# Optimization experiments

Hardware: AMD Instinct MI355X
Metric: run time of the kernel (lower is better)

Reference implementation:

```python
import jax, jax.numpy as jnp
import numpy as np

E = 8      # num_experts
A = 128    # angle feature size = input_size - 4
TGT = 3    # target size
HID = 16   # expert MLP hidden / latent / main GRU hidden
OUT = 128  # motion decoder output size
B = 64
W = 128
F = A + TGT + 1  # 132
BN_EPS = 1e-5


def _gru_layer(x, Wih, Whh, bih, bhh):
    # x: (B, T, I); Wih: (3H, I); Whh: (3H, H). PyTorch GRU equations.
    xW = jnp.einsum('bti,gi->btg', x, Wih) + bih  # precompute input gates (B,T,3H)
    H = Whh.shape[1]

    def step(h, xw):
        gh = h @ Whh.T + bhh
        ir, iz, inn = jnp.split(xw, 3, axis=-1)
        hr, hz, hn = jnp.split(gh, 3, axis=-1)
        r = jax.nn.sigmoid(ir + hr)
        z = jax.nn.sigmoid(iz + hz)
        n = jnp.tanh(inn + r * hn)
        h_new = (1.0 - z) * n + z * h
        return h_new, h_new

    h0 = jnp.zeros((x.shape[0], H), x.dtype)
    _, ys = jax.lax.scan(step, h0, jnp.swapaxes(xW, 0, 1))
    return jnp.swapaxes(ys, 0, 1)  # (B, T, H)


def _expert_mlp(x, om, w1, b1, w2, b2, g, bt):
    # Blend expert weights per-sample, then matvec; fused as one einsum (same math).
    h = jnp.einsum('bi,be,eih->bh', x, om, w1) + om @ b1
    # BatchNorm1d, training-mode batch statistics (biased variance), then ELU
    m = h.mean(0)
    v = h.var(0)
    h = jax.nn.elu(g * (h - m) * jax.lax.rsqrt(v + BN_EPS) + bt)
    return jnp.einsum('bh,be,eho->bo', h, om, w2) + om @ b2


def _forward(Local, Remote,
             gW_ih0, gW_hh0, gb_ih0, gb_hh0, gW_ih1, gW_hh1, gb_ih1, gb_hh1,
             ae_w1, ae_b1, ae_w2, ae_b2, ae_g, ae_bt,
             md_w1, md_b1, md_w2, md_b2, md_g, md_bt,
             mW_ih0, mW_hh0, mb_ih0, mb_hh0, mW_ih1, mW_hh1, mb_ih1, mb_hh1):
    Bn, Wn, _ = Local.shape
    LA = Local[..., :A]
    RA = Remote[..., :A]
    LT = Local[..., A:A + TGT]
    RT = Remote[..., A:A + TGT]
    Scale = Remote[..., A + TGT]  # (B, W)

    def gate(t):
        h = _gru_layer(t, gW_ih0, gW_hh0, gb_ih0, gb_hh0)
        h = _gru_layer(h, gW_ih1, gW_hh1, gb_ih1, gb_hh1)
        return jax.nn.softmax(h, axis=-1)

    Lo = gate(LT)  # (B, W, E)
    Ro = gate(RT)

    ZL = _expert_mlp(LA.reshape(-1, A), Lo.reshape(-1, E), ae_w1, ae_b1, ae_w2, ae_b2, ae_g, ae_bt)
    ZR = _expert_mlp(RA.reshape(-1, A), Ro.reshape(-1, E), ae_w1, ae_b1, ae_w2, ae_b2, ae_g, ae_bt)
    Z = (ZL + ZR).reshape(Bn, Wn, HID)

    Z = _gru_layer(Z, mW_ih0, mW_hh0, mb_ih0, mb_hh0)
    Z = _gru_layer(Z, mW_ih1, mW_hh1, mb_ih1, mb_hh1)
    Z = Z[:, -1]  # (B, HID)

    dec_in = jnp.concatenate([Z, Scale[:, -1:]], axis=-1)  # (B, HID+1)
    return _expert_mlp(dec_in, Ro[:, -1], md_w1, md_b1, md_w2, md_b2, md_g, md_bt)


def setup_inputs() -> dict:
    key = jax.random.key(0)
    ks = iter(jax.random.split(key, 40))

    def u(shape, bound):
        return jax.random.uniform(next(ks), shape, jnp.float32, -bound, bound)

    d = {}
    d['Local'] = jax.random.normal(next(ks), (B, W, F), jnp.float32)
    d['Remote'] = jax.random.normal(next(ks), (B, W, F), jnp.float32)

    def gru_params(pref, isz, hsz):
        bd = 1.0 / np.sqrt(hsz)
        d[pref + 'W_ih0'] = u((3 * hsz, isz), bd)
        d[pref + 'W_hh0'] = u((3 * hsz, hsz), bd)
        d[pref + 'b_ih0'] = u((3 * hsz,), bd)
        d[pref + 'b_hh0'] = u((3 * hsz,), bd)
        d[pref + 'W_ih1'] = u((3 * hsz, hsz), bd)
        d[pref + 'W_hh1'] = u((3 * hsz, hsz), bd)
        d[pref + 'b_ih1'] = u((3 * hsz,), bd)
        d[pref + 'b_hh1'] = u((3 * hsz,), bd)

    gru_params('g', TGT, E)    # gating GRU: 2 layers, hidden = num_experts
    gru_params('m', HID, HID)  # main GRU: 2 layers, hidden = 16

    def expert(pref, isz, hsz, osz):
        b1 = float(np.sqrt(6.0 / (isz * hsz)))
        b2 = float(np.sqrt(6.0 / (hsz * osz)))
        d[pref + '_w1'] = u((E, isz, hsz), b1)
        d[pref + '_b1'] = jnp.zeros((E, hsz), jnp.float32)
        d[pref + '_w2'] = u((E, hsz, osz), b2)
        d[pref + '_b2'] = jnp.zeros((E, osz), jnp.float32)
        d[pref + '_g'] = jnp.ones((hsz,), jnp.float32)
        d[pref + '_bt'] = jnp.zeros((hsz,), jnp.float32)

    expert('ae', A, HID, HID)        # angle encoder
    expert('md', HID + 1, HID, OUT)  # motion decoder
    return d


def reference(Local, Remote,
              gW_ih0, gW_hh0, gb_ih0, gb_hh0, gW_ih1, gW_hh1, gb_ih1, gb_hh1,
              ae_w1, ae_b1, ae_w2, ae_b2, ae_g, ae_bt,
              md_w1, md_b1, md_w2, md_b2, md_g, md_bt,
              mW_ih0, mW_hh0, mb_ih0, mb_hh0, mW_ih1, mW_hh1, mb_ih1, mb_hh1):
    return _forward(Local, Remote,
                    gW_ih0, gW_hh0, gb_ih0, gb_hh0, gW_ih1, gW_hh1, gb_ih1, gb_hh1,
                    ae_w1, ae_b1, ae_w2, ae_b2, ae_g, ae_bt,
                    md_w1, md_b1, md_w2, md_b2, md_g, md_bt,
                    mW_ih0, mW_hh0, mb_ih0, mb_hh0, mW_ih1, mW_hh1, mb_ih1, mb_hh1)
```

## Files before the change

### kernel.cpp

```cpp
#include <hip/hip_runtime.h>
#include <cstdint>
#include <cstddef>

#define DEV __device__ __forceinline__

typedef float f2 __attribute__((ext_vector_type(2)));

constexpr float L2E = 1.4426950408889634f;
constexpr float T2E = 2.8853900817779268f;

DEV float readlanef(float v, int l) {
    return __uint_as_float(__builtin_amdgcn_readlane(__float_as_uint(v), l));
}
DEV float fsig2(float y)  { return __builtin_amdgcn_rcpf(1.0f + __builtin_amdgcn_exp2f(-y)); }
DEV float ftanh2(float y) { return 1.0f - 2.0f * __builtin_amdgcn_rcpf(1.0f + __builtin_amdgcn_exp2f(y)); }

constexpr size_t ACC   = 0;
constexpr size_t LO    = 128;
constexpr size_t RO    = LO + 65536;
constexpr size_t HBUF  = RO + 65536;
constexpr size_t ZLAST = HBUF + 262144;

__global__ __launch_bounds__(64, 1) void k1_gate(
    const float* __restrict__ Local, const float* __restrict__ Remote,
    const float* __restrict__ Wih0, const float* __restrict__ Whh0,
    const float* __restrict__ bih0, const float* __restrict__ bhh0,
    const float* __restrict__ Wih1, const float* __restrict__ Whh1,
    const float* __restrict__ bih1, const float* __restrict__ bhh1,
    float* __restrict__ ws)
{
    const int tid = threadIdx.x;
    const int j = tid & 7;
    const int layer = (tid >> 3) & 1;
    const int blk = blockIdx.x;
    const int track = blk >> 6;
    const int b = blk & 63;
    if (blk == 0) ws[ACC + tid] = 0.f;

    __shared__ float xwg[128][24];
    __shared__ float h1all[128][9];

    const float* __restrict__ src = track ? Remote : Local;
    for (int t = tid; t < 128; t += 64) {
        const float* p = src + ((size_t)b * 128 + t) * 132 + 128;
        float x0 = p[0], x1 = p[1], x2 = p[2];
#pragma unroll
        for (int u = 0; u < 24; ++u) {
            float a = bih0[u];
            a = fmaf(Wih0[u * 3 + 0], x0, a);
            a = fmaf(Wih0[u * 3 + 1], x1, a);
            a = fmaf(Wih0[u * 3 + 2], x2, a);
            xwg[t][u] = a * (u < 16 ? L2E : T2E);
        }
    }

    const float* __restrict__ Wlo = layer ? Wih1 : Whh0;
    const float mhi = layer ? 1.f : 0.f;
    const float m0f = layer ? 0.f : 1.f;
    f2 wr2[8], wz2[8], wc2[8];
#pragma unroll
    for (int m = 0; m < 4; ++m) {
        wr2[m].x = L2E * Wlo[j * 8 + 2 * m];
        wr2[m].y = L2E * Wlo[j * 8 + 2 * m + 1];
        wz2[m].x = L2E * Wlo[(8 + j) * 8 + 2 * m];
        wz2[m].y = L2E * Wlo[(8 + j) * 8 + 2 * m + 1];
        wc2[m].x = T2E * Wlo[(16 + j) * 8 + 2 * m];
        wc2[m].y = T2E * Wlo[(16 + j) * 8 + 2 * m + 1];
        wr2[4 + m].x = mhi * L2E * Whh1[j * 8 + 2 * m];
        wr2[4 + m].y = mhi * L2E * Whh1[j * 8 + 2 * m + 1];
        wz2[4 + m].x = mhi * L2E * Whh1[(8 + j) * 8 + 2 * m];
        wz2[4 + m].y = mhi * L2E * Whh1[(8 + j) * 8 + 2 * m + 1];
        wc2[4 + m].x = mhi * T2E * Whh1[(16 + j) * 8 + 2 * m];
        wc2[4 + m].y = mhi * T2E * Whh1[(16 + j) * 8 + 2 * m + 1];
    }
    const float base_r  = L2E * (layer ? (bih1[j] + bhh1[j])         : bhh0[j]);
    const float base_z  = L2E * (layer ? (bih1[8 + j] + bhh1[8 + j]) : bhh0[8 + j]);
    const float base_in = T2E * (layer ? bih1[16 + j]                : 0.f);
    const float base_dn = T2E * (layer ? bhh1[16 + j]                : bhh0[16 + j]);
    __syncthreads();

    float hown = 0.f;
    float p0 = xwg[0][j], p1 = xwg[0][8 + j], p2 = xwg[0][16 + j];
#pragma unroll 1
    for (int t = 0; t <= 128; ++t) {
        int tn = t < 127 ? t + 1 : 127;
        float q0 = xwg[tn][j], q1 = xwg[tn][8 + j], q2 = xwg[tn][16 + j];
        f2 vb2[8];
#pragma unroll
        for (int m = 0; m < 8; ++m) {
            vb2[m].x = readlanef(hown, 2 * m);
            vb2[m].y = readlanef(hown, 2 * m + 1);
        }
        f2 srE = wr2[0] * vb2[0], srO = wr2[1] * vb2[1];
        f2 szE = wz2[0] * vb2[0], szO = wz2[1] * vb2[1];
#pragma unroll
        for (int m = 2; m < 8; m += 2) {
            srE += wr2[m] * vb2[m];     srO += wr2[m + 1] * vb2[m + 1];
            szE += wz2[m] * vb2[m];     szO += wz2[m + 1] * vb2[m + 1];
        }
        f2 scA = wc2[0] * vb2[0], scB = wc2[1] * vb2[1];
        f2 scC = wc2[4] * vb2[4], scD = wc2[5] * vb2[5];
#pragma unroll
        for (int m = 2; m < 4; m += 2) {
            scA += wc2[m] * vb2[m];     scB += wc2[m + 1] * vb2[m + 1];
            scC += wc2[4 + m] * vb2[4 + m]; scD += wc2[5 + m] * vb2[5 + m];
        }
        f2 sr = srE + srO, sz = szE + szO;
        f2 scL = scA + scB, scH = scC + scD;
        float ar = fmaf(m0f, p0, base_r) + sr.x + sr.y;
        float az = fmaf(m0f, p1, base_z) + sz.x + sz.y;
        float ac_lo = scL.x + scL.y;
        float ac_hi = scH.x + scH.y;
        float r = fsig2(ar);
        float z = fsig2(az);
        float in_ = layer ? (base_in + ac_lo) : p2;
        float dn  = base_dn + (layer ? ac_hi : ac_lo);
        float n = ftanh2(fmaf(r, dn, in_));
        float hnew = fmaf(z, hown - n, n);
        bool act = layer ? (t >= 1) : (t < 128);
        hown = act ? hnew : hown;
        if (tid >= 8 && tid < 16) h1all[t ? t - 1 : 0][j] = hown;
        p0 = q0; p1 = q1; p2 = q2;
    }
    __syncthreads();

    float* __restrict__ outp = ws + (track ? RO : LO);
    for (int t = tid; t < 128; t += 64) {
        float vv[8];
#pragma unroll
        for (int k = 0; k < 8; ++k) vv[k] = h1all[t][k];
        float mx = vv[0];
#pragma unroll
        for (int k = 1; k < 8; ++k) mx = fmaxf(mx, vv[k]);
        float ssum = 0.f;
#pragma unroll
        for (int k = 0; k < 8; ++k) { vv[k] = __expf(vv[k] - mx); ssum += vv[k]; }
        float inv = __builtin_amdgcn_rcpf(ssum);
        size_t base = ((size_t)b * 128 + t) * 8;
        float4 o0 = make_float4(vv[0] * inv, vv[1] * inv, vv[2] * inv, vv[3] * inv);
        float4 o1 = make_float4(vv[4] * inv, vv[5] * inv, vv[6] * inv, vv[7] * inv);
        *(float4*)(outp + base) = o0;
        *(float4*)(outp + base + 4) = o1;
    }
}

__global__ __launch_bounds__(256) void k2_expert1(
    const float* __restrict__ Local, const float* __restrict__ Remote,
    const float* __restrict__ ae_w1, const float* __restrict__ ae_b1,
    float* __restrict__ ws)
{
    const int blk = blockIdx.x;
    const int track = blk >> 7;
    const int n0 = (blk & 127) * 64;
    const float* __restrict__ X = track ? Remote : Local;
    const float* __restrict__ om = ws + (track ? RO : LO);

    __shared__ __align__(16) float xsh[64 * 132];
    __shared__ __align__(16) float wsh[16 * 1060];
    __shared__ float omsh[64][8];
    __shared__ float b1sh[128];
    __shared__ float red[32];
    const int tid = threadIdx.x;

    for (int i = tid; i < 2048; i += 256) {
        int r = i >> 5, q = i & 31;
        ((float4*)&xsh[r * 132])[q] = ((const float4*)(X + (size_t)(n0 + r) * 132))[q];
    }
    for (int i4 = tid; i4 < 4096; i4 += 256) {
        float4 v = ((const float4*)ae_w1)[i4];
        int i = i4 * 4;
#pragma unroll
        for (int c = 0; c < 4; ++c) {
            int ii = i + c;
            int h = ii & 15, kk = (ii >> 4) & 127, e = ii >> 11;
            float vc = c == 0 ? v.x : c == 1 ? v.y : c == 2 ? v.z : v.w;
            wsh[h * 1060 + e * 132 + kk] = vc;
        }
    }
    for (int i = tid; i < 512; i += 256) omsh[i >> 3][i & 7] = om[(size_t)(n0 + (i >> 3)) * 8 + (i & 7)];
    for (int i = tid; i < 128; i += 256) b1sh[i] = ae_b1[i];
    if (tid < 32) red[tid] = 0.f;
    __syncthreads();

    const int hh = tid & 15, rg = tid >> 4;
    float acc[4][8];
#pragma unroll
    for (int r = 0; r < 4; ++r)
#pragma unroll
        for (int e = 0; e < 8; ++e) acc[r][e] = 0.f;

#pragma unroll 4
    for (int kq = 0; kq < 32; ++kq) {
        float4 xv[4], wv[8];
#pragma unroll
        for (int r = 0; r < 4; ++r) xv[r] = *(const float4*)&xsh[(rg * 4 + r) * 132 + kq * 4];
#pragma unroll
        for (int e = 0; e < 8; ++e) wv[e] = *(const float4*)&wsh[hh * 1060 + e * 132 + kq * 4];
#pragma unroll
        for (int r = 0; r < 4; ++r)
#pragma unroll
            for (int e = 0; e < 8; ++e) {
                float a = acc[r][e];
                a = fmaf(xv[r].x, wv[e].x, a);
                a = fmaf(xv[r].y, wv[e].y, a);
                a = fmaf(xv[r].z, wv[e].z, a);
                a = fmaf(xv[r].w, wv[e].w, a);
                acc[r][e] = a;
            }
    }

    float s = 0.f, s2 = 0.f;
    float* __restrict__ hout = ws + HBUF + (size_t)track * 131072;
#pragma unroll
    for (int r = 0; r < 4; ++r) {
        int row = rg * 4 + r;
        float hv = 0.f;
#pragma unroll
        for (int e = 0; e < 8; ++e) hv = fmaf(omsh[row][e], acc[r][e] + b1sh[e * 16 + hh], hv);
        hout[(size_t)(n0 + row) * 16 + hh] = hv;
        s += hv; s2 += hv * hv;
    }
    __syncthreads();
    atomicAdd(&red[hh], s);
    atomicAdd(&red[16 + hh], s2);
    __syncthreads();
    if (tid < 32) atomicAdd(&ws[ACC + track * 32 + tid], red[tid]);
}

__global__ __launch_bounds__(256, 1) void k34_fused(
    const float* __restrict__ ae_w2, const float* __restrict__ ae_b2,
    const float* __restrict__ ae_g, const float* __restrict__ ae_bt,
    const float* __restrict__ mWih0, const float* __restrict__ mbih0,
    const float* __restrict__ Whh0, const float* __restrict__ bhh0,
    const float* __restrict__ Wih1, const float* __restrict__ Whh1,
    const float* __restrict__ bih1, const float* __restrict__ bhh1,
    float* __restrict__ ws)
{
    const int s = blockIdx.x;
    const int tid = threadIdx.x;

    __shared__ float stat[4][16];
    __shared__ float omsh[2][128][8];
    __shared__ __align__(16) float w2t[16 * 132];
    __shared__ float b2sh[128];
    __shared__ __align__(16) float actsh[2][128][16];
    __shared__ __align__(16) float zsh[128][20];
    __shared__ __align__(16) float wihsh[48][20];
    __shared__ float bihsh[48];
    __shared__ float xwsh[128 * 48];

    if (tid < 32) {
        int trk = tid >> 4, h = tid & 15;
        float sm = ws[ACC + trk * 32 + h], s2 = ws[ACC + trk * 32 + 16 + h];
        float m = sm * (1.f / 8192.f);
        float v = fmaxf(s2 * (1.f / 8192.f) - m * m, 0.f);
        stat[trk * 2][h] = m;
        stat[trk * 2 + 1][h] = rsqrtf(v + 1e-5f);
    }
    for (int i = tid; i < 2048; i += 256) {
        int e = i >> 8, h = (i >> 4) & 15, o = i & 15;
        w2t[o * 132 + e * 16 + h] = ae_w2[i];
    }
    for (int i = tid; i < 128; i += 256) b2sh[i] = ae_b2[i];
    for (int i = tid; i < 768; i += 256) wihsh[i >> 4][i & 15] = mWih0[i];
    if (tid < 48) bihsh[tid] = mbih0[tid];
    for (int i = tid; i < 2048; i += 256) {
        int trk = i >> 10, r = (i >> 3) & 127, e = i & 7;
        omsh[trk][r][e] = ws[(trk ? RO : LO) + ((size_t)s * 128 + r) * 8 + e];
    }
    __syncthreads();

    for (int i = tid; i < 4096; i += 256) {
        int trk = i >> 11, r = (i >> 4) & 127, h = i & 15;
        float v = ws[HBUF + (size_t)trk * 131072 + ((size_t)s * 128 + r) * 16 + h];
        float a = ae_g[h] * (v - stat[trk * 2][h]) * stat[trk * 2 + 1][h] + ae_bt[h];
        actsh[trk][r][h] = a > 0.f ? a : expm1f(a);
    }
    __syncthreads();

    {
        const int o = tid & 15, rb = tid >> 4;
        float zacc[8];
#pragma unroll
        for (int r8 = 0; r8 < 8; ++r8) zacc[r8] = 0.f;
#pragma unroll
        for (int ec = 0; ec < 2; ++ec) {
            float4 wv[4][4];
#pragma unroll
            for (int e4 = 0; e4 < 4; ++e4)
#pragma unroll
                for (int q = 0; q < 4; ++q)
                    wv[e4][q] = *(const float4*)&w2t[o * 132 + (ec * 4 + e4) * 16 + q * 4];
#pragma unroll
            for (int r8 = 0; r8 < 8; ++r8) {
                int r = rb * 8 + r8;
#pragma unroll
                for (int trk = 0; trk < 2; ++trk) {
                    float4 av[4];
#pragma unroll
                    for (int q = 0; q < 4; ++q) av[q] = *(const float4*)&actsh[trk][r][q * 4];
#pragma unroll
                    for (int e4 = 0; e4 < 4; ++e4) {
                        int e = ec * 4 + e4;
                        float t = b2sh[e * 16 + o];
                        t = fmaf(av[0].x, wv[e4][0].x, t);
                        t = fmaf(av[0].y, wv[e4][0].y, t);
                        t = fmaf(av[0].z, wv[e4][0].z, t);
                        t = fmaf(av[0].w, wv[e4][0].w, t);
                        t = fmaf(av[1].x, wv[e4][1].x, t);
                        t = fmaf(av[1].y, wv[e4][1].y, t);
                        t = fmaf(av[1].z, wv[e4][1].z, t);
                        t = fmaf(av[1].w, wv[e4][1].w, t);
                        t = fmaf(av[2].x, wv[e4][2].x, t);
                        t = fmaf(av[2].y, wv[e4][2].y, t);
                        t = fmaf(av[2].z, wv[e4][2].z, t);
                        t = fmaf(av[2].w, wv[e4][2].w, t);
                        t = fmaf(av[3].x, wv[e4][3].x, t);
                        t = fmaf(av[3].y, wv[e4][3].y, t);
                        t = fmaf(av[3].z, wv[e4][3].z, t);
                        t = fmaf(av[3].w, wv[e4][3].w, t);
                        zacc[r8] = fmaf(omsh[trk][r][e], t, zacc[r8]);
                    }
                }
            }
        }
#pragma unroll
        for (int r8 = 0; r8 < 8; ++r8) zsh[rb * 8 + r8][o] = zacc[r8];
    }
    __syncthreads();

    {
        const int r = tid >> 1, gh = (tid & 1) * 24;
        float4 zv[4];
#pragma unroll
        for (int q = 0; q < 4; ++q) zv[q] = *(const float4*)&zsh[r][q * 4];
#pragma unroll
        for (int gg = 0; gg < 24; ++gg) {
            int g = gh + gg;
            float a = bihsh[g];
#pragma unroll
            for (int q = 0; q < 4; ++q) {
                float4 wv = *(const float4*)&wihsh[g][q * 4];
                a = fmaf(zv[q].x, wv.x, a);
                a = fmaf(zv[q].y, wv.y, a);
                a = fmaf(zv[q].z, wv.z, a);
                a = fmaf(zv[q].w, wv.w, a);
            }
            xwsh[r * 48 + g] = a * (g < 32 ? L2E : T2E);
        }
    }
    __syncthreads();

    if (tid >= 64) return;

    const int j = tid & 15;
    const int layer = (tid >> 4) & 1;

    const float* __restrict__ Wlo = layer ? Wih1 : Whh0;
    const float mhi = layer ? 1.f : 0.f;
    const float m0f = layer ? 0.f : 1.f;
    f2 wr2[16], wz2[16], wc2[16];
#pragma unroll
    for (int m = 0; m < 8; ++m) {
        wr2[m].x = L2E * Wlo[j * 16 + 2 * m];
        wr2[m].y = L2E * Wlo[j * 16 + 2 * m + 1];
        wz2[m].x = L2E * Wlo[(16 + j) * 16 + 2 * m];
        wz2[m].y = L2E * Wlo[(16 + j) * 16 + 2 * m + 1];
        wc2[m].x = T2E * Wlo[(32 + j) * 16 + 2 * m];
        wc2[m].y = T2E * Wlo[(32 + j) * 16 + 2 * m + 1];
        wr2[8 + m].x = mhi * L2E * Whh1[j * 16 + 2 * m];
        wr2[8 + m].y = mhi * L2E * Whh1[j * 16 + 2 * m + 1];
        wz2[8 + m].x = mhi * L2E * Whh1[(16 + j) * 16 + 2 * m];
        wz2[8 + m].y = mhi * L2E * Whh1[(16 + j) * 16 + 2 * m + 1];
        wc2[8 + m].x = mhi * T2E * Whh1[(32 + j) * 16 + 2 * m];
        wc2[8 + m].y = mhi * T2E * Whh1[(32 + j) * 16 + 2 * m + 1];
    }
    const float base_r  = L2E * (layer ? (bih1[j] + bhh1[j])           : bhh0[j]);
    const float base_z  = L2E * (layer ? (bih1[16 + j] + bhh1[16 + j]) : bhh0[16 + j]);
    const float base_in = T2E * (layer ? bih1[32 + j]                  : 0.f);
    const float base_dn = T2E * (layer ? bhh1[32 + j]                  : bhh0[32 + j]);

    float hown = 0.f;
    float p0 = xwsh[j], p1 = xwsh[16 + j], p2 = xwsh[32 + j];
#pragma unroll 1
    for (int t = 0; t <= 128; ++t) {
        int tn = (t < 127 ? t + 1 : 127) * 48;
        float q0 = xwsh[tn + j], q1 = xwsh[tn + 16 + j], q2 = xwsh[tn + 32 + j];
        f2 vb2[16];
#pragma unroll
        for (int m = 0; m < 16; ++m) {
            vb2[m].x = readlanef(hown, 2 * m);
            vb2[m].y = readlanef(hown, 2 * m + 1);
        }
        f2 srE = wr2[0] * vb2[0], srO = wr2[1] * vb2[1];
        f2 szE = wz2[0] * vb2[0], szO = wz2[1] * vb2[1];
#pragma unroll
        for (int m = 2; m < 16; m += 2) {
            srE += wr2[m] * vb2[m];     srO += wr2[m + 1] * vb2[m + 1];
            szE += wz2[m] * vb2[m];     szO += wz2[m + 1] * vb2[m + 1];
        }
        f2 scA = wc2[0] * vb2[0], scB = wc2[1] * vb2[1];
        f2 scC = wc2[8] * vb2[8], scD = wc2[9] * vb2[9];
#pragma unroll
        for (int m = 2; m < 8; m += 2) {
            scA += wc2[m] * vb2[m];         scB += wc2[m + 1] * vb2[m + 1];
            scC += wc2[8 + m] * vb2[8 + m]; scD += wc2[9 + m] * vb2[9 + m];
        }
        f2 sr = srE + srO, sz = szE + szO;
        f2 scL = scA + scB, scH = scC + scD;
        float ar = fmaf(m0f, p0, base_r) + sr.x + sr.y;
        float az = fmaf(m0f, p1, base_z) + sz.x + sz.y;
        float ac_lo = scL.x + scL.y;
        float ac_hi = scH.x + scH.y;
        float r = fsig2(ar);
        float z = fsig2(az);
        float in_ = layer ? (base_in + ac_lo) : p2;
        float dn  = base_dn + (layer ? ac_hi : ac_lo);
        float n = ftanh2(fmaf(r, dn, in_));
        float hnew = fmaf(z, hown - n, n);
        bool act = layer ? (t >= 1) : (t < 128);
        hown = act ? hnew : hown;
        p0 = q0; p1 = q1; p2 = q2;
    }
    if (tid >= 16 && tid < 32) ws[ZLAST + (size_t)s * 16 + j] = hown;
}

__global__ __launch_bounds__(256) void k5_dec(
    const float* __restrict__ Remote,
    const float* __restrict__ md_w1, const float* __restrict__ md_b1,
    const float* __restrict__ md_g, const float* __restrict__ md_bt,
    const float* __restrict__ md_w2, const float* __restrict__ md_b2,
    const float* __restrict__ ws, float* __restrict__ out)
{
    const int o0 = blockIdx.x * 8;
    const int tid = threadIdx.x;
    __shared__ float xsh[64][17];
    __shared__ float omsh[64][8];
    __shared__ float w1sh[2176];
    __shared__ float b1sh[128];
    __shared__ float hsh[64][17];
    __shared__ float ssum[16], ss2[16], mstat[2][16];
    __shared__ float ash[64][17];
    __shared__ float w2sh[8][16][8];
    __shared__ float b2sh[8][8];

    for (int i = tid; i < 1024; i += 256) xsh[i >> 4][i & 15] = ws[ZLAST + i];
    if (tid < 64) xsh[tid][16] = Remote[((size_t)tid * 128 + 127) * 132 + 131];
    for (int i = tid; i < 512; i += 256)
        omsh[i >> 3][i & 7] = ws[RO + ((size_t)(i >> 3) * 128 + 127) * 8 + (i & 7)];
    for (int i = tid; i < 2176; i += 256) w1sh[i] = md_w1[i];
    for (int i = tid; i < 128; i += 256) b1sh[i] = md_b1[i];
    for (int i = tid; i < 1024; i += 256) {
        int e = i >> 7, h = (i >> 3) & 15, oo = i & 7;
        w2sh[e][h][oo] = md_w2[((size_t)e * 16 + h) * 128 + o0 + oo];
    }
    if (tid < 64) b2sh[tid >> 3][tid & 7] = md_b2[(size_t)(tid >> 3) * 128 + o0 + (tid & 7)];
    if (tid < 16) { ssum[tid] = 0.f; ss2[tid] = 0.f; }
    __syncthreads();

    for (int i = tid; i < 1024; i += 256) {
        int b = i >> 4, h = i & 15;
        float accv = 0.f;
#pragma unroll
        for (int e = 0; e < 8; ++e) {
            float t = b1sh[e * 16 + h];
            const float* w = &w1sh[e * 272 + h];
#pragma unroll
            for (int i2 = 0; i2 < 17; ++i2) t = fmaf(xsh[b][i2], w[i2 * 16], t);
            accv = fmaf(omsh[b][e], t, accv);
        }
        hsh[b][h] = accv;
        atomicAdd(&ssum[h], accv);
        atomicAdd(&ss2[h], accv * accv);
    }
    __syncthreads();
    if (tid < 16) {
        float m = ssum[tid] * (1.f / 64.f);
        float v = fmaxf(ss2[tid] * (1.f / 64.f) - m * m, 0.f);
        mstat[0][tid] = m;
        mstat[1][tid] = rsqrtf(v + 1e-5f);
    }
    __syncthreads();
    for (int i = tid; i < 1024; i += 256) {
        int b = i >> 4, h = i & 15;
        float a = md_g[h] * (hsh[b][h] - mstat[0][h]) * mstat[1][h] + md_bt[h];
        ash[b][h] = a > 0.f ? a : expm1f(a);
    }
    __syncthreads();

    for (int i = tid; i < 512; i += 256) {
        int b = i >> 3, oo = i & 7;
        float accv = 0.f;
#pragma unroll
        for (int e = 0; e < 8; ++e) {
            float t = b2sh[e][oo];
#pragma unroll
            for (int h = 0; h < 16; ++h) t = fmaf(ash[b][h], w2sh[e][h][oo], t);
            accv = fmaf(omsh[b][e], t, accv);
        }
        out[(size_t)b * 128 + o0 + oo] = accv;
    }
}

extern "C" void kernel_launch(void* const* d_in, const int* in_sizes, int n_in,
                              void* d_out, int out_size, void* d_ws, size_t ws_size,
                              hipStream_t stream) {
    const float* Local  = (const float*)d_in[0];
    const float* Remote = (const float*)d_in[1];
    const float* gWih0  = (const float*)d_in[2];
    const float* gWhh0  = (const float*)d_in[3];
    const float* gbih0  = (const float*)d_in[4];
    const float* gbhh0  = (const float*)d_in[5];
    const float* gWih1  = (const float*)d_in[6];
    const float* gWhh1  = (const float*)d_in[7];
    const float* gbih1  = (const float*)d_in[8];
    const float* gbhh1  = (const float*)d_in[9];
    const float* mWih0  = (const float*)d_in[10];
    const float* mWhh0  = (const float*)d_in[11];
    const float* mbih0  = (const float*)d_in[12];
    const float* mbhh0  = (const float*)d_in[13];
    const float* mWih1  = (const float*)d_in[14];
    const float* mWhh1  = (const float*)d_in[15];
    const float* mbih1  = (const float*)d_in[16];
    const float* mbhh1  = (const float*)d_in[17];
    const float* ae_w1  = (const float*)d_in[18];
    const float* ae_b1  = (const float*)d_in[19];
    const float* ae_w2  = (const float*)d_in[20];
    const float* ae_b2  = (const float*)d_in[21];
    const float* ae_g   = (const float*)d_in[22];
    const float* ae_bt  = (const float*)d_in[23];
    const float* md_w1  = (const float*)d_in[24];
    const float* md_b1  = (const float*)d_in[25];
    const float* md_w2  = (const float*)d_in[26];
    const float* md_b2  = (const float*)d_in[27];
    const float* md_g   = (const float*)d_in[28];
    const float* md_bt  = (const float*)d_in[29];
    float* ws  = (float*)d_ws;
    float* out = (float*)d_out;

    k1_gate<<<128, 64, 0, stream>>>(Local, Remote, gWih0, gWhh0, gbih0, gbhh0,
                                    gWih1, gWhh1, gbih1, gbhh1, ws);
    k2_expert1<<<256, 256, 0, stream>>>(Local, Remote, ae_w1, ae_b1, ws);
    k34_fused<<<64, 256, 0, stream>>>(ae_w2, ae_b2, ae_g, ae_bt, mWih0, mbih0,
                                      mWhh0, mbhh0, mWih1, mWhh1, mbih1, mbhh1, ws);
    k5_dec<<<16, 256, 0, stream>>>(Remote, md_w1, md_b1, md_g, md_bt,
                                   md_w2, md_b2, ws, out);
}
```

Before: 228.0 us.

## Split fused encoder+GRU kernel into parallel phase and wavefront recurrence kernel

Splits the fused k34 kernel into two kernels. The first is a wide 256-block phase that computes the expert second layer and the main GRU input projections and stores them to a new workspace region. The second is a 64-thread recurrence kernel that runs both GRU layers skewed by one step in a single wave, sharing hidden state via readlane. The aim is to spread the non-recurrent work across more CUs and shorten the serial recurrence, at the cost of an extra launch and an extra global round-trip. The new path only runs when the workspace is large enough; otherwise the old fused kernel is used.

```diff
diff --git a/kernel.cpp b/kernel.cpp
--- a/kernel.cpp
+++ b/kernel.cpp
@@ -20,6 +20,8 @@
 constexpr size_t RO    = LO + 65536;
 constexpr size_t HBUF  = RO + 65536;
 constexpr size_t ZLAST = HBUF + 262144;
+constexpr size_t XW    = ZLAST + 1024;
+constexpr size_t WS_NEED = XW + 393216;
 
 __global__ __launch_bounds__(64, 1) void k1_gate(
     const float* __restrict__ Local, const float* __restrict__ Remote,
@@ -225,6 +227,216 @@
     atomicAdd(&red[16 + hh], s2);
     __syncthreads();
     if (tid < 32) atomicAdd(&ws[ACC + track * 32 + tid], red[tid]);
+}
+
+__global__ __launch_bounds__(256) void k3_phaseA(
+    const float* __restrict__ ae_w2, const float* __restrict__ ae_b2,
+    const float* __restrict__ ae_g, const float* __restrict__ ae_bt,
+    const float* __restrict__ mWih0, const float* __restrict__ mbih0,
+    float* __restrict__ ws)
+{
+    const int blk = blockIdx.x;
+    const int s = blk >> 2;
+    const int r0 = (blk & 3) * 32;
+    const int tid = threadIdx.x;
+
+    __shared__ float stat[4][16];
+    __shared__ __align__(16) float w2t[16 * 132];
+    __shared__ float b2sh[128];
+    __shared__ float omsh[2][32][8];
+    __shared__ __align__(16) float actsh[2][32][16];
+    __shared__ __align__(16) float zsh[32][20];
+    __shared__ __align__(16) float wihsh[48][20];
+    __shared__ float bihsh[48];
+
+    if (tid < 32) {
+        int trk = tid >> 4, h = tid & 15;
+        float sm = ws[ACC + trk * 32 + h], s2 = ws[ACC + trk * 32 + 16 + h];
+        float m = sm * (1.f / 8192.f);
+        float v = fmaxf(s2 * (1.f / 8192.f) - m * m, 0.f);
+        stat[trk * 2][h] = m;
+        stat[trk * 2 + 1][h] = rsqrtf(v + 1e-5f);
+    }
+    for (int i = tid; i < 2048; i += 256) {
+        int e = i >> 8, h = (i >> 4) & 15, o = i & 15;
+        w2t[o * 132 + e * 16 + h] = ae_w2[i];
+    }
+    for (int i = tid; i < 128; i += 256) b2sh[i] = ae_b2[i];
+    for (int i = tid; i < 768; i += 256) wihsh[i >> 4][i & 15] = mWih0[i];
+    if (tid < 48) bihsh[tid] = mbih0[tid];
+    for (int i = tid; i < 512; i += 256) {
+        int trk = i >> 8, r = (i >> 3) & 31, e = i & 7;
+        omsh[trk][r][e] = ws[(trk ? RO : LO) + ((size_t)s * 128 + r0 + r) * 8 + e];
+    }
+    __syncthreads();
+
+    for (int i = tid; i < 1024; i += 256) {
+        int trk = i >> 9, r = (i >> 4) & 31, h = i & 15;
+        float v = ws[HBUF + (size_t)trk * 131072 + ((size_t)s * 128 + r0 + r) * 16 + h];
+        float a = ae_g[h] * (v - stat[trk * 2][h]) * stat[trk * 2 + 1][h] + ae_bt[h];
+        actsh[trk][r][h] = a > 0.f ? a : expm1f(a);
+    }
+    __syncthreads();
+
+    {
+        const int o = tid & 15, rb = tid >> 4;
+        float zacc[2] = {0.f, 0.f};
+#pragma unroll
+        for (int ec = 0; ec < 2; ++ec) {
+            float4 wv[4][4];
+            float bo[4];
+#pragma unroll
+            for (int e4 = 0; e4 < 4; ++e4) {
+                bo[e4] = b2sh[(ec * 4 + e4) * 16 + o];
+#pragma unroll
+                for (int q = 0; q < 4; ++q)
+                    wv[e4][q] = *(const float4*)&w2t[o * 132 + (ec * 4 + e4) * 16 + q * 4];
+            }
+#pragma unroll
+            for (int r2 = 0; r2 < 2; ++r2) {
+                int r = rb * 2 + r2;
+#pragma unroll
+                for (int trk = 0; trk < 2; ++trk) {
+                    float4 av[4];
+#pragma unroll
+                    for (int q = 0; q < 4; ++q) av[q] = *(const float4*)&actsh[trk][r][q * 4];
+#pragma unroll
+                    for (int e4 = 0; e4 < 4; ++e4) {
+                        int e = ec * 4 + e4;
+                        float t = bo[e4];
+                        t = fmaf(av[0].x, wv[e4][0].x, t);
+                        t = fmaf(av[0].y, wv[e4][0].y, t);
+                        t = fmaf(av[0].z, wv[e4][0].z, t);
+                        t = fmaf(av[0].w, wv[e4][0].w, t);
+                        t = fmaf(av[1].x, wv[e4][1].x, t);
+                        t = fmaf(av[1].y, wv[e4][1].y, t);
+                        t = fmaf(av[1].z, wv[e4][1].z, t);
+                        t = fmaf(av[1].w, wv[e4][1].w, t);
+                        t = fmaf(av[2].x, wv[e4][2].x, t);
+                        t = fmaf(av[2].y, wv[e4][2].y, t);
+                        t = fmaf(av[2].z, wv[e4][2].z, t);
+                        t = fmaf(av[2].w, wv[e4][2].w, t);
+                        t = fmaf(av[3].x, wv[e4][3].x, t);
+                        t = fmaf(av[3].y, wv[e4][3].y, t);
+                        t = fmaf(av[3].z, wv[e4][3].z, t);
+                        t = fmaf(av[3].w, wv[e4][3].w, t);
+                        zacc[r2] = fmaf(omsh[trk][r][e], t, zacc[r2]);
+                    }
+                }
+            }
+        }
+#pragma unroll
+        for (int r2 = 0; r2 < 2; ++r2) zsh[rb * 2 + r2][o] = zacc[r2];
+    }
+    __syncthreads();
+
+    {
+        const int r = tid >> 3, g0 = (tid & 7) * 6;
+        float4 zv[4];
+#pragma unroll
+        for (int q = 0; q < 4; ++q) zv[q] = *(const float4*)&zsh[r][q * 4];
+        float* __restrict__ xwp = ws + XW + ((size_t)s * 128 + r0 + r) * 48;
+#pragma unroll
+        for (int gg = 0; gg < 6; ++gg) {
+            int g = g0 + gg;
+            float a = bihsh[g];
+#pragma unroll
+            for (int q = 0; q < 4; ++q) {
+                float4 wv = *(const float4*)&wihsh[g][q * 4];
+                a = fmaf(zv[q].x, wv.x, a);
+                a = fmaf(zv[q].y, wv.y, a);
+                a = fmaf(zv[q].z, wv.z, a);
+                a = fmaf(zv[q].w, wv.w, a);
+            }
+            xwp[g] = a * (g < 32 ? L2E : T2E);
+        }
+    }
+}
+
+__global__ __launch_bounds__(64, 1) void k4_rec(
+    const float* __restrict__ Whh0, const float* __restrict__ bhh0,
+    const float* __restrict__ Wih1, const float* __restrict__ Whh1,
+    const float* __restrict__ bih1, const float* __restrict__ bhh1,
+    float* __restrict__ ws)
+{
+    const int s = blockIdx.x;
+    const int tid = threadIdx.x;
+    __shared__ __align__(16) float xwsh[128 * 48];
+
+    const float4* __restrict__ xwg = (const float4*)(ws + XW + (size_t)s * 6144);
+    for (int i = tid; i < 1536; i += 64) ((float4*)xwsh)[i] = xwg[i];
+
+    const int j = tid & 15;
+    const int layer = (tid >> 4) & 1;
+
+    const float* __restrict__ Wlo = layer ? Wih1 : Whh0;
+    const float mhi = layer ? 1.f : 0.f;
+    const float m0f = layer ? 0.f : 1.f;
+    f2 wr2[16], wz2[16], wc2[16];
+#pragma unroll
+    for (int m = 0; m < 8; ++m) {
+        wr2[m].x = L2E * Wlo[j * 16 + 2 * m];
+        wr2[m].y = L2E * Wlo[j * 16 + 2 * m + 1];
+        wz2[m].x = L2E * Wlo[(16 + j) * 16 + 2 * m];
+        wz2[m].y = L2E * Wlo[(16 + j) * 16 + 2 * m + 1];
+        wc2[m].x = T2E * Wlo[(32 + j) * 16 + 2 * m];
+        wc2[m].y = T2E * Wlo[(32 + j) * 16 + 2 * m + 1];
+        wr2[8 + m].x = mhi * L2E * Whh1[j * 16 + 2 * m];
+        wr2[8 + m].y = mhi * L2E * Whh1[j * 16 + 2 * m + 1];
+        wz2[8 + m].x = mhi * L2E * Whh1[(16 + j) * 16 + 2 * m];
+        wz2[8 + m].y = mhi * L2E * Whh1[(16 + j) * 16 + 2 * m + 1];
+        wc2[8 + m].x = mhi * T2E * Whh1[(32 + j) * 16 + 2 * m];
+        wc2[8 + m].y = mhi * T2E * Whh1[(32 + j) * 16 + 2 * m + 1];
+    }
+    const float base_r  = L2E * (layer ? (bih1[j] + bhh1[j])           : bhh0[j]);
+    const float base_z  = L2E * (layer ? (bih1[16 + j] + bhh1[16 + j]) : bhh0[16 + j]);
+    const float base_in = T2E * (layer ? bih1[32 + j]                  : 0.f);
+    const float base_dn = T2E * (layer ? bhh1[32 + j]                  : bhh0[32 + j]);
+    __syncthreads();
+
+    float hown = 0.f;
+    float p0 = xwsh[j], p1 = xwsh[16 + j], p2 = xwsh[32 + j];
+#pragma unroll 1
+    for (int t = 0; t <= 128; ++t) {
+        int tn = (t < 127 ? t + 1 : 127) * 48;
+        float q0 = xwsh[tn + j], q1 = xwsh[tn + 16 + j], q2 = xwsh[tn + 32 + j];
+        f2 vb2[16];
+#pragma unroll
+        for (int m = 0; m < 16; ++m) {
+            vb2[m].x = readlanef(hown, 2 * m);
+            vb2[m].y = readlanef(hown, 2 * m + 1);
+        }
+        f2 srE = wr2[0] * vb2[0], srO = wr2[1] * vb2[1];
+        f2 szE = wz2[0] * vb2[0], szO = wz2[1] * vb2[1];
+#pragma unroll
+        for (int m = 2; m < 16; m += 2) {
+            srE += wr2[m] * vb2[m];     srO += wr2[m + 1] * vb2[m + 1];
+            szE += wz2[m] * vb2[m];     szO += wz2[m + 1] * vb2[m + 1];
+        }
+        f2 scA = wc2[0] * vb2[0], scB = wc2[1] * vb2[1];
+        f2 scC = wc2[8] * vb2[8], scD = wc2[9] * vb2[9];
+#pragma unroll
+        for (int m = 2; m < 8; m += 2) {
+            scA += wc2[m] * vb2[m];         scB += wc2[m + 1] * vb2[m + 1];
+            scC += wc2[8 + m] * vb2[8 + m]; scD += wc2[9 + m] * vb2[9 + m];
+        }
+        f2 sr = srE + srO, sz = szE + szO;
+        f2 scL = scA + scB, scH = scC + scD;
+        float ar = fmaf(m0f, p0, base_r) + sr.x + sr.y;
+        float az = fmaf(m0f, p1, base_z) + sz.x + sz.y;
+        float ac_lo = scL.x + scL.y;
+        float ac_hi = scH.x + scH.y;
+        float r = fsig2(ar);
+        float z = fsig2(az);
+        float in_ = layer ? (base_in + ac_lo) : p2;
+        float dn  = base_dn + (layer ? ac_hi : ac_lo);
+        float n = ftanh2(fmaf(r, dn, in_));
+        float hnew = fmaf(z, hown - n, n);
+        bool act = layer ? (t >= 1) : (t < 128);
+        hown = act ? hnew : hown;
+        p0 = q0; p1 = q1; p2 = q2;
+    }
+    if (tid >= 16 && tid < 32) ws[ZLAST + (size_t)s * 16 + j] = hown;
 }
 
 __global__ __launch_bounds__(256, 1) void k34_fused(
@@ -541,8 +753,13 @@
     k1_gate<<<128, 64, 0, stream>>>(Local, Remote, gWih0, gWhh0, gbih0, gbhh0,
                                     gWih1, gWhh1, gbih1, gbhh1, ws);
     k2_expert1<<<256, 256, 0, stream>>>(Local, Remote, ae_w1, ae_b1, ws);
-    k34_fused<<<64, 256, 0, stream>>>(ae_w2, ae_b2, ae_g, ae_bt, mWih0, mbih0,
-                                      mWhh0, mbhh0, mWih1, mWhh1, mbih1, mbhh1, ws);
+    if (ws_size >= WS_NEED * sizeof(float)) {
+        k3_phaseA<<<256, 256, 0, stream>>>(ae_w2, ae_b2, ae_g, ae_bt, mWih0, mbih0, ws);
+        k4_rec<<<64, 64, 0, stream>>>(mWhh0, mbhh0, mWih1, mWhh1, mbih1, mbhh1, ws);
+    } else {
+        k34_fused<<<64, 256, 0, stream>>>(ae_w2, ae_b2, ae_g, ae_bt, mWih0, mbih0,
+                                          mWhh0, mbhh0, mWih1, mWhh1, mbih1, mbhh1, ws);
+    }
     k5_dec<<<16, 256, 0, stream>>>(Remote, md_w1, md_b1, md_g, md_bt,
                                    md_w2, md_b2, ws, out);
 }
```

Result: no change. 227.9 us (-0.1%).
